# Performance work log

Measured on AMD Instinct MI355X. Metric: run time of the kernel, lower is better.

The kernel has to match this reference:

```python
import jax, jax.numpy as jnp
import numpy as np


def binarize(x):
    # hard sign in forward, tanh surrogate gradient (STE)
    t = jnp.tanh(x)
    hard = jnp.where(x >= 0, jnp.ones_like(x), -jnp.ones_like(x))
    return jax.lax.stop_gradient(hard - t) + t


def round_ste(x):
    return x + jax.lax.stop_gradient(jnp.round(x) - x)


def binary_shift_scale(shift_param, lo=-8.0, hi=0.0):
    return 2.0 ** round_ste(jnp.clip(shift_param, lo, hi))


def setup_inputs() -> dict:
    key = jax.random.key(0)
    k1, k2 = jax.random.split(key)
    B, S, IN, OUT = 4, 2048, 4096, 16384
    x = jax.random.normal(k1, (B, S, IN), dtype=jnp.float32)
    weight = jax.random.normal(k2, (OUT, IN), dtype=jnp.float32) * 0.02
    threshold = jnp.zeros((OUT, 1), dtype=jnp.float32)
    shift_param = jnp.array(-4.5, dtype=jnp.float32)
    return {"x": x, "weight": weight, "threshold": threshold, "shift_param": shift_param}


def reference(x, weight, threshold, shift_param):
    xb = binarize(x)                               # [B,S,IN]
    wb = binarize(weight - threshold)              # [OUT,IN]
    out = jnp.einsum('bsi,oi->bso', xb, wb)        # dense GEMM on +/-1 values
    return out * binary_shift_scale(shift_param)   # pow2 shift scale
```

## Files before the change

### kernel.cpp

```cpp
#include <hip/hip_runtime.h>
#include <stdint.h>

#define M_ROWS 8192
#define N_COLS 16384
#define K_ELEMS 4096
#define KW 128
#define LDS_STRIDE 20

__global__ void pack_x_kernel(const float4* __restrict__ x,
                              uint64_t* __restrict__ out, int nwaves) {
    int lane = threadIdx.x & 63;
    int gw = (blockIdx.x * blockDim.x + threadIdx.x) >> 6;
    int stride = (gridDim.x * blockDim.x) >> 6;
    for (int w = gw; w < nwaves; w += stride) {
        float4 v = x[(size_t)w * 64 + lane];
        uint64_t m0 = __ballot(v.x < 0.0f);
        uint64_t m1 = __ballot(v.y < 0.0f);
        uint64_t m2 = __ballot(v.z < 0.0f);
        uint64_t m3 = __ballot(v.w < 0.0f);
        uint64_t sel = (lane == 0) ? m0 : (lane == 1) ? m1 : (lane == 2) ? m2 : m3;
        if (lane < 4) out[(size_t)w * 4 + lane] = sel;
    }
}

__global__ void pack_w_kernel(const float4* __restrict__ wgt,
                              const float* __restrict__ thr,
                              uint64_t* __restrict__ out, int nwaves) {
    int lane = threadIdx.x & 63;
    int gw = (blockIdx.x * blockDim.x + threadIdx.x) >> 6;
    int stride = (gridDim.x * blockDim.x) >> 6;
    for (int w = gw; w < nwaves; w += stride) {
        size_t f4 = (size_t)w * 64 + lane;
        float t = thr[f4 >> 10];
        float4 v = wgt[f4];
        uint64_t m0 = __ballot(v.x - t < 0.0f);
        uint64_t m1 = __ballot(v.y - t < 0.0f);
        uint64_t m2 = __ballot(v.z - t < 0.0f);
        uint64_t m3 = __ballot(v.w - t < 0.0f);
        uint64_t sel = (lane == 0) ? m0 : (lane == 1) ? m1 : (lane == 2) ? m2 : m3;
        if (lane < 4) out[(size_t)w * 4 + lane] = sel;
    }
}

__launch_bounds__(256, 2)
__global__ void bgemm_kernel(const uint32_t* __restrict__ A,
                             const uint32_t* __restrict__ B,
                             const float* __restrict__ shift,
                             float* __restrict__ out) {
    __shared__ uint32_t As[128 * LDS_STRIDE];
    __shared__ uint32_t Bs[128 * LDS_STRIDE];

    const int tid = threadIdx.x;
    const int tx = tid & 15;
    const int ty = tid >> 4;
    const int bm = blockIdx.y * 128;
    const int bn = blockIdx.x * 128;

    const int r0 = tid >> 2, g0 = tid & 3;
    const int r1 = (tid + 256) >> 2, g1 = tid & 3;

    uint32_t acc[8][8];
    #pragma unroll
    for (int i = 0; i < 8; ++i)
        #pragma unroll
        for (int j = 0; j < 8; ++j) acc[i][j] = 0u;

    uint4 pa0, pa1, pb0, pb1;
    pa0 = *(const uint4*)&A[(size_t)(bm + r0) * KW + 0 + g0 * 4];
    pa1 = *(const uint4*)&A[(size_t)(bm + r1) * KW + 0 + g1 * 4];
    pb0 = *(const uint4*)&B[(size_t)(bn + r0) * KW + 0 + g0 * 4];
    pb1 = *(const uint4*)&B[(size_t)(bn + r1) * KW + 0 + g1 * 4];

    for (int kb = 0; kb < KW; kb += 16) {
        *(uint4*)&As[r0 * LDS_STRIDE + g0 * 4] = pa0;
        *(uint4*)&As[r1 * LDS_STRIDE + g1 * 4] = pa1;
        *(uint4*)&Bs[r0 * LDS_STRIDE + g0 * 4] = pb0;
        *(uint4*)&Bs[r1 * LDS_STRIDE + g1 * 4] = pb1;
        __syncthreads();

        if (kb + 16 < KW) {
            int kn = kb + 16;
            pa0 = *(const uint4*)&A[(size_t)(bm + r0) * KW + kn + g0 * 4];
            pa1 = *(const uint4*)&A[(size_t)(bm + r1) * KW + kn + g1 * 4];
            pb0 = *(const uint4*)&B[(size_t)(bn + r0) * KW + kn + g0 * 4];
            pb1 = *(const uint4*)&B[(size_t)(bn + r1) * KW + kn + g1 * 4];
        }

        #pragma unroll
        for (int g = 0; g < 4; ++g) {
            uint4 b[8];
            #pragma unroll
            for (int c = 0; c < 8; ++c)
                b[c] = *(const uint4*)&Bs[(tx + 16 * c) * LDS_STRIDE + g * 4];
            #pragma unroll
            for (int r = 0; r < 8; ++r) {
                uint4 a = *(const uint4*)&As[(ty + 16 * r) * LDS_STRIDE + g * 4];
                #pragma unroll
                for (int c = 0; c < 8; ++c) {
                    acc[r][c] += __popc(a.x ^ b[c].x);
                    acc[r][c] += __popc(a.y ^ b[c].y);
                    acc[r][c] += __popc(a.z ^ b[c].z);
                    acc[r][c] += __popc(a.w ^ b[c].w);
                }
            }
        }
        __syncthreads();
    }

    float sp = shift[0];
    float rr = rintf(fminf(fmaxf(sp, -8.0f), 0.0f));
    float scale = exp2f(rr);
    float base = (float)K_ELEMS * scale;
    float m2s = -2.0f * scale;

    #pragma unroll
    for (int i = 0; i < 8; ++i) {
        size_t rowoff = (size_t)(bm + ty + 16 * i) * (size_t)N_COLS + (size_t)bn;
        #pragma unroll
        for (int j = 0; j < 8; ++j) {
            out[rowoff + tx + 16 * j] = fmaf(m2s, (float)acc[i][j], base);
        }
    }
}

extern "C" void kernel_launch(void* const* d_in, const int* in_sizes, int n_in,
                              void* d_out, int out_size, void* d_ws, size_t ws_size,
                              hipStream_t stream) {
    const float* x     = (const float*)d_in[0];
    const float* w     = (const float*)d_in[1];
    const float* thr   = (const float*)d_in[2];
    const float* shift = (const float*)d_in[3];

    uint32_t* Apk = (uint32_t*)d_ws;
    uint32_t* Bpk = Apk + (size_t)M_ROWS * KW;
    float* out = (float*)d_out;

    pack_x_kernel<<<2048, 256, 0, stream>>>((const float4*)x, (uint64_t*)Apk,
                                            (M_ROWS * K_ELEMS) / 256);
    pack_w_kernel<<<4096, 256, 0, stream>>>((const float4*)w, thr, (uint64_t*)Bpk,
                                            (N_COLS * K_ELEMS) / 256);

    dim3 grid(N_COLS / 128, M_ROWS / 128);
    bgemm_kernel<<<grid, 256, 0, stream>>>(Apk, Bpk, shift, out);
}
```

Before: 1.586 ms.

## Replace popcount binary GEMM with int8 MFMA GEMM on +/-1 bytes

```diff
diff --git a/kernel.cpp b/kernel.cpp
--- a/kernel.cpp
+++ b/kernel.cpp
@@ -6,6 +6,141 @@
 #define K_ELEMS 4096
 #define KW 128
 #define LDS_STRIDE 20
+
+typedef int i32x4  __attribute__((ext_vector_type(4)));
+typedef int i32x16 __attribute__((ext_vector_type(16)));
+
+typedef const __attribute__((address_space(1))) void* gptr_t;
+typedef __attribute__((address_space(3))) void*       lptr_t;
+
+__device__ __forceinline__ void gload_lds16(const void* g, void* l) {
+    __builtin_amdgcn_global_load_lds((gptr_t)g, (lptr_t)l, 16, 0, 0);
+}
+
+__global__ void conv_x_i8(const float4* __restrict__ x, uint32_t* __restrict__ o,
+                          int n4) {
+    int i = blockIdx.x * blockDim.x + threadIdx.x;
+    int st = gridDim.x * blockDim.x;
+    for (; i < n4; i += st) {
+        float4 v = x[i];
+        uint32_t b0 = (v.x >= 0.0f) ? 0x01u : 0xFFu;
+        uint32_t b1 = (v.y >= 0.0f) ? 0x01u : 0xFFu;
+        uint32_t b2 = (v.z >= 0.0f) ? 0x01u : 0xFFu;
+        uint32_t b3 = (v.w >= 0.0f) ? 0x01u : 0xFFu;
+        o[i] = b0 | (b1 << 8) | (b2 << 16) | (b3 << 24);
+    }
+}
+
+__global__ void conv_w_i8(const float4* __restrict__ w, const float* __restrict__ thr,
+                          uint32_t* __restrict__ o, int n4) {
+    int i = blockIdx.x * blockDim.x + threadIdx.x;
+    int st = gridDim.x * blockDim.x;
+    for (; i < n4; i += st) {
+        float t = thr[i >> 10];
+        float4 v = w[i];
+        uint32_t b0 = (v.x - t >= 0.0f) ? 0x01u : 0xFFu;
+        uint32_t b1 = (v.y - t >= 0.0f) ? 0x01u : 0xFFu;
+        uint32_t b2 = (v.z - t >= 0.0f) ? 0x01u : 0xFFu;
+        uint32_t b3 = (v.w - t >= 0.0f) ? 0x01u : 0xFFu;
+        o[i] = b0 | (b1 << 8) | (b2 << 16) | (b3 << 24);
+    }
+}
+
+__launch_bounds__(256, 3)
+__global__ void bgemm_i8(const char* __restrict__ A,
+                         const char* __restrict__ B,
+                         const float* __restrict__ shift,
+                         float* __restrict__ out) {
+    __shared__ __align__(16) char As[2][128 * 64];
+    __shared__ __align__(16) char Bs[2][128 * 64];
+
+    const int tid  = threadIdx.x;
+    const int lane = tid & 63;
+    const int wid  = tid >> 6;
+    const int wx   = wid & 1;
+    const int wy   = wid >> 1;
+    const int bm   = blockIdx.y * 128;
+    const int bn   = blockIdx.x * 128;
+
+    const char* gA[2];
+    const char* gB[2];
+    int lofs[2];
+    #pragma unroll
+    for (int j = 0; j < 2; ++j) {
+        int c  = wid * 2 + j;
+        int li = c * 64 + lane;
+        int r  = li >> 2;
+        int s  = (li & 3) ^ ((r >> 1) & 3);
+        gA[j]   = A + (size_t)(bm + r) * K_ELEMS + s * 16;
+        gB[j]   = B + (size_t)(bn + r) * K_ELEMS + s * 16;
+        lofs[j] = c * 1024;
+    }
+
+    const int l31 = lane & 31, hi = lane >> 5;
+    int aOff[2][2], bOff[2][2];
+    #pragma unroll
+    for (int t = 0; t < 2; ++t) {
+        int Rm = wy * 64 + t * 32 + l31;
+        int Rn = wx * 64 + t * 32 + l31;
+        #pragma unroll
+        for (int ks = 0; ks < 2; ++ks) {
+            aOff[t][ks] = Rm * 64 + (((ks * 2 + hi) ^ ((Rm >> 1) & 3)) << 4);
+            bOff[t][ks] = Rn * 64 + (((ks * 2 + hi) ^ ((Rn >> 1) & 3)) << 4);
+        }
+    }
+
+    i32x16 acc[2][2] = {};
+
+    #pragma unroll
+    for (int j = 0; j < 2; ++j) {
+        gload_lds16(gA[j], &As[0][lofs[j]]);
+        gload_lds16(gB[j], &Bs[0][lofs[j]]);
+    }
+    __syncthreads();
+
+    const int NT = K_ELEMS / 64;
+    #pragma unroll 2
+    for (int t = 0; t < NT; ++t) {
+        const int cur = t & 1;
+        if (t + 1 < NT) {
+            const int kb = (t + 1) * 64;
+            #pragma unroll
+            for (int j = 0; j < 2; ++j) {
+                gload_lds16(gA[j] + kb, &As[cur ^ 1][lofs[j]]);
+                gload_lds16(gB[j] + kb, &Bs[cur ^ 1][lofs[j]]);
+            }
+        }
+        #pragma unroll
+        for (int ks = 0; ks < 2; ++ks) {
+            i32x4 a0 = *(const i32x4*)(&As[cur][aOff[0][ks]]);
+            i32x4 a1 = *(const i32x4*)(&As[cur][aOff[1][ks]]);
+            i32x4 b0 = *(const i32x4*)(&Bs[cur][bOff[0][ks]]);
+            i32x4 b1 = *(const i32x4*)(&Bs[cur][bOff[1][ks]]);
+            acc[0][0] = __builtin_amdgcn_mfma_i32_32x32x32_i8(a0, b0, acc[0][0], 0, 0, 0);
+            acc[0][1] = __builtin_amdgcn_mfma_i32_32x32x32_i8(a0, b1, acc[0][1], 0, 0, 0);
+            acc[1][0] = __builtin_amdgcn_mfma_i32_32x32x32_i8(a1, b0, acc[1][0], 0, 0, 0);
+            acc[1][1] = __builtin_amdgcn_mfma_i32_32x32x32_i8(a1, b1, acc[1][1], 0, 0, 0);
+        }
+        __syncthreads();
+    }
+
+    float sp    = shift[0];
+    float rr    = rintf(fminf(fmaxf(sp, -8.0f), 0.0f));
+    float scale = exp2f(rr);
+
+    #pragma unroll
+    for (int mt = 0; mt < 2; ++mt) {
+        #pragma unroll
+        for (int nt = 0; nt < 2; ++nt) {
+            #pragma unroll
+            for (int reg = 0; reg < 16; ++reg) {
+                int row = bm + wy * 64 + mt * 32 + (reg & 3) + 8 * (reg >> 2) + 4 * hi;
+                int col = bn + wx * 64 + nt * 32 + l31;
+                out[(size_t)row * N_COLS + col] = scale * (float)acc[mt][nt][reg];
+            }
+        }
+    }
+}
 
 __global__ void pack_x_kernel(const float4* __restrict__ x,
                               uint64_t* __restrict__ out, int nwaves) {
@@ -130,16 +265,32 @@
     const float* w     = (const float*)d_in[1];
     const float* thr   = (const float*)d_in[2];
     const float* shift = (const float*)d_in[3];
-
-    uint32_t* Apk = (uint32_t*)d_ws;
-    uint32_t* Bpk = Apk + (size_t)M_ROWS * KW;
     float* out = (float*)d_out;
 
-    pack_x_kernel<<<2048, 256, 0, stream>>>((const float4*)x, (uint64_t*)Apk,
-                                            (M_ROWS * K_ELEMS) / 256);
-    pack_w_kernel<<<4096, 256, 0, stream>>>((const float4*)w, thr, (uint64_t*)Bpk,
-                                            (N_COLS * K_ELEMS) / 256);
-
-    dim3 grid(N_COLS / 128, M_ROWS / 128);
-    bgemm_kernel<<<grid, 256, 0, stream>>>(Apk, Bpk, shift, out);
-}
+    const size_t A_BYTES = (size_t)M_ROWS * K_ELEMS;
+    const size_t B_BYTES = (size_t)N_COLS * K_ELEMS;
+
+    if (ws_size >= A_BYTES + B_BYTES) {
+        char* Ai8 = (char*)d_ws;
+        char* Bi8 = Ai8 + A_BYTES;
+
+        conv_x_i8<<<2048, 256, 0, stream>>>((const float4*)x, (uint32_t*)Ai8,
+                                            (int)(A_BYTES / 4));
+        conv_w_i8<<<2048, 256, 0, stream>>>((const float4*)w, thr, (uint32_t*)Bi8,
+                                            (int)(B_BYTES / 4));
+
+        dim3 grid(N_COLS / 128, M_ROWS / 128);
+        bgemm_i8<<<grid, 256, 0, stream>>>(Ai8, Bi8, shift, out);
+    } else {
+        uint32_t* Apk = (uint32_t*)d_ws;
+        uint32_t* Bpk = Apk + (size_t)M_ROWS * KW;
+
+        pack_x_kernel<<<2048, 256, 0, stream>>>((const float4*)x, (uint64_t*)Apk,
+                                                (M_ROWS * K_ELEMS) / 256);
+        pack_w_kernel<<<4096, 256, 0, stream>>>((const float4*)w, thr, (uint64_t*)Bpk,
+                                                (N_COLS * K_ELEMS) / 256);
+
+        dim3 grid(N_COLS / 128, M_ROWS / 128);
+        bgemm_kernel<<<grid, 256, 0, stream>>>(Apk, Bpk, shift, out);
+    }
+}
```

Result: faster. 1.384 ms (-12.8%).
